# Kernel tuning notes

Measured on AMD Instinct MI355X. Metric: run time of the kernel, lower is better.

## Reference

```python
import jax, jax.numpy as jnp
import numpy as np

B, N, F, K = 16384, 64, 128, 64


def setup_inputs() -> dict:
    key = jax.random.key(0)
    kx, kd = jax.random.split(key)
    x = jax.random.normal(kx, (B, F), dtype=jnp.float32)
    D = jax.random.normal(kd, (N, F, K), dtype=jnp.float32)  # per-cluster factor dictionaries
    return {"x": x, "D": D}


def reference(x, D):
    # --- assignment step (torch.no_grad in original) ---
    # Dtx[n,b,j] = sum_i D[n,i,j] * x[b,i]
    Dtx = jnp.einsum('nij,bi->nbj', D, x)                      # [N,B,K]
    # per-cluster (D^T D)^{-1}, batched inverse over the cluster axis
    DTD = jnp.einsum('nij,nik->njk', D, D)                     # [N,K,K]
    DTD_inv = jnp.linalg.inv(DTD)                              # [N,K,K]
    Cs = jnp.einsum('nbj,nkj->nbk', Dtx, DTD_inv)              # [N,B,K]
    x_hat = jnp.einsum('nij,nbj->nbi', D, Cs)                  # [N,B,F]
    # nearest-subspace assignment per sample
    label = jnp.argmin(jnp.linalg.norm(x_hat - x[None], axis=-1), axis=0)  # [B] int
    C = Cs[label, jnp.arange(x.shape[0])]                      # [B,K] gather per sample
    # --- reconstruction loss: sum_i || x[i] - D[label[i]] @ C[i] ||^2 ---
    x_rec = jnp.einsum('bik,bk->bi', D[label], C)              # grouped gather + matmul
    se_loss = jnp.sum(jnp.square(x - x_rec))
    return se_loss, label
```

## Files before the change

### kernel.cpp

```cpp
#include <hip/hip_runtime.h>
#include <hip/hip_bf16.h>

#define B_N 16384
#define TAU 0.25f
#define GS 68
#define YS 132
#define DS 68

typedef float f32x4 __attribute__((ext_vector_type(4)));
typedef short s16x8 __attribute__((ext_vector_type(8)));

__device__ __forceinline__ void gl_lds16(const void* g, void* l) {
    __builtin_amdgcn_global_load_lds(
        (const __attribute__((address_space(1))) void*)g,
        (__attribute__((address_space(3))) void*)l, 16, 0, 0);
}

__device__ __forceinline__ unsigned short bf16_bits(float v) {
    __hip_bfloat16 h = __float2bfloat16(v);
    return *reinterpret_cast<unsigned short*>(&h);
}

__device__ __forceinline__ float readlane_f(float v, int l) {
    return __int_as_float(__builtin_amdgcn_readlane(__float_as_int(v), l));
}

__global__ __launch_bounds__(512) void prep_convert(const float* __restrict__ x,
                                                    const float* __restrict__ D,
                                                    unsigned short* __restrict__ xh,
                                                    float* __restrict__ nrm,
                                                    float* __restrict__ Qg,
                                                    unsigned short* __restrict__ Bht,
                                                    float* __restrict__ out) {
    const int t = threadIdx.x;

    if (blockIdx.x >= 64) {
        const int gid = (blockIdx.x - 64) * 512 + t;
        if (gid == 0) out[0] = 0.0f;
        const size_t base = (size_t)gid * 32;
        float s = 0.0f;
        #pragma unroll
        for (int c = 0; c < 8; ++c) {
            const f32x4 v = ((const f32x4*)(x + base))[c];
            s += v.x * v.x + v.y * v.y + v.z * v.z + v.w * v.w;
            ushort4 h;
            h.x = bf16_bits(v.x); h.y = bf16_bits(v.y);
            h.z = bf16_bits(v.z); h.w = bf16_bits(v.w);
            ((ushort4*)(xh + base))[c] = h;
        }
        s += __shfl_xor(s, 1, 64);
        s += __shfl_xor(s, 2, 64);
        if ((gid & 3) == 0) nrm[gid >> 2] = s;
        return;
    }

    __shared__ float Y[64 * YS];
    __shared__ __align__(16) float Dl[128 * DS];
    __shared__ __align__(16) float G[64 * GS + 64];
    __shared__ __align__(16) float Lti[8 * 8 * 8];
    const int n = blockIdx.x;
    const float* Dn = D + (size_t)n * 8192;

    for (int e4 = t; e4 < 2048; e4 += 512) {
        const int c = e4 >> 4, j4 = (e4 & 15) * 4;
        const f32x4 v = ((const f32x4*)Dn)[e4];
        *(f32x4*)&Dl[c * DS + j4] = v;
        Y[(j4 + 0) * YS + c] = v.x;
        Y[(j4 + 1) * YS + c] = v.y;
        Y[(j4 + 2) * YS + c] = v.z;
        Y[(j4 + 3) * YS + c] = v.w;
    }
    __syncthreads();

    {
        const int h = t >> 8;
        const int a0 = (t & 15) * 4, b0 = ((t >> 4) & 15) * 4;
        const int i0 = h * 64;
        float acc[4][4] = {};
        #pragma unroll 4
        for (int i = i0; i < i0 + 64; ++i) {
            const f32x4 av = *(const f32x4*)&Dl[i * DS + a0];
            const f32x4 bv = *(const f32x4*)&Dl[i * DS + b0];
            const float aa[4] = {av.x, av.y, av.z, av.w};
            const float bb[4] = {bv.x, bv.y, bv.z, bv.w};
            #pragma unroll
            for (int p = 0; p < 4; ++p)
                #pragma unroll
                for (int q = 0; q < 4; ++q) acc[p][q] = fmaf(aa[p], bb[q], acc[p][q]);
        }
        if (h == 0) {
            #pragma unroll
            for (int p = 0; p < 4; ++p)
                #pragma unroll
                for (int q = 0; q < 4; ++q) G[(a0 + p) * GS + b0 + q] = acc[p][q];
        }
        __syncthreads();
        if (h == 1) {
            #pragma unroll
            for (int p = 0; p < 4; ++p)
                #pragma unroll
                for (int q = 0; q < 4; ++q) G[(a0 + p) * GS + b0 + q] += acc[p][q];
        }
    }
    __syncthreads();

    #pragma unroll
    for (int p8 = 0; p8 < 8; ++p8) {
        const int pb = p8 * 8;
        if (t < 64) {
            const int lane = t;
            const f32x4 v0 = *(const f32x4*)&G[lane * GS + pb];
            const f32x4 v1 = *(const f32x4*)&G[lane * GS + pb + 4];
            float g[8] = {v0.x, v0.y, v0.z, v0.w, v1.x, v1.y, v1.z, v1.w};
            #pragma unroll
            for (int kk = 0; kk < 8; ++kk) {
                const int k = pb + kk;
                const float dk = readlane_f(g[kk], k);
                const float rinv = 1.0f / sqrtf(dk);
                const float lik = g[kk] * rinv;
                g[kk] = lik;
                if (lane == 0) G[64 * GS + k] = rinv;
                #pragma unroll
                for (int jj = kk + 1; jj < 8; ++jj) {
                    const float ljk = readlane_f(lik, pb + jj);
                    g[jj] -= lik * ljk;
                }
            }
            *(f32x4*)&G[lane * GS + pb]     = (f32x4){g[0], g[1], g[2], g[3]};
            *(f32x4*)&G[lane * GS + pb + 4] = (f32x4){g[4], g[5], g[6], g[7]};
        }
        __syncthreads();
        const int base = pb + 8;
        if (base < 64) {
            for (int i = base + (t >> 5); i < 64; i += 16) {
                const f32x4 Li0 = *(const f32x4*)&G[i * GS + pb];
                const f32x4 Li1 = *(const f32x4*)&G[i * GS + pb + 4];
                for (int j = base + (t & 31); j < 64; j += 32) {
                    const f32x4 Lj0 = *(const f32x4*)&G[j * GS + pb];
                    const f32x4 Lj1 = *(const f32x4*)&G[j * GS + pb + 4];
                    float s = G[i * GS + j];
                    s -= Li0.x * Lj0.x + Li0.y * Lj0.y + Li0.z * Lj0.z + Li0.w * Lj0.w;
                    s -= Li1.x * Lj1.x + Li1.y * Lj1.y + Li1.z * Lj1.z + Li1.w * Lj1.w;
                    G[i * GS + j] = s;
                }
            }
        }
        __syncthreads();
    }

    if (t < 64) {
        const int bi = t >> 3, c = t & 7;
        const int base = bi * 8;
        float m[8];
        #pragma unroll
        for (int r = 0; r < 8; ++r) {
            float s = (r == c) ? 1.0f : 0.0f;
            #pragma unroll
            for (int k = 0; k < r; ++k)
                s -= G[(base + r) * GS + base + k] * m[k];
            m[r] = s * G[64 * GS + base + r];
        }
        #pragma unroll
        for (int r = 0; r < 8; ++r) Lti[(base + r) * 8 + c] = m[r];
    }
    __syncthreads();

    {
        const int j = t >> 3, r = t & 7, jb = j >> 3;
        const float rinvj = G[64 * GS + j];
        for (int m8 = 0; m8 < 8; ++m8) {
            if (m8 >= jb) {
                const int g = m8 * 8 + r;
                float wv = (g == j) ? 1.0f : 0.0f;
                if (m8 > jb) {
                    #pragma unroll
                    for (int kk = 0; kk < 8; ++kk) {
                        const int gp = jb * 8 + kk;
                        const float liv = (gp > j) ? G[j * GS + gp]
                                         : ((gp == j) ? rinvj : 0.0f);
                        wv -= G[g * GS + gp] * liv;
                    }
                    for (int mm = jb + 1; mm < m8; ++mm) {
                        const f32x4 Lg0 = *(const f32x4*)&G[g * GS + mm * 8];
                        const f32x4 Lg1 = *(const f32x4*)&G[g * GS + mm * 8 + 4];
                        const f32x4 Mv0 = *(const f32x4*)&G[j * GS + mm * 8];
                        const f32x4 Mv1 = *(const f32x4*)&G[j * GS + mm * 8 + 4];
                        wv = fmaf(-Lg0.x, Mv0.x, wv);
                        wv = fmaf(-Lg0.y, Mv0.y, wv);
                        wv = fmaf(-Lg0.z, Mv0.z, wv);
                        wv = fmaf(-Lg0.w, Mv0.w, wv);
                        wv = fmaf(-Lg1.x, Mv1.x, wv);
                        wv = fmaf(-Lg1.y, Mv1.y, wv);
                        wv = fmaf(-Lg1.z, Mv1.z, wv);
                        wv = fmaf(-Lg1.w, Mv1.w, wv);
                    }
                }
                float z = 0.0f;
                #pragma unroll
                for (int rp = 0; rp < 8; ++rp) {
                    const float wrp = __shfl(wv, (t & 56) | rp, 64);
                    z = fmaf(Lti[g * 8 + rp], wrp, z);
                }
                if (g > j) G[j * GS + g] = z;
            }
            __syncthreads();
        }
    }

    {
        const int jj = t >> 5;
        const int jz = (jj & 1) ? (15 - (jj >> 1)) : (jj >> 1);
        const int j0 = jz * 4, c0 = (t & 31) * 4;
        const f32x4 rv4 = *(const f32x4*)&G[64 * GS + j0];
        float acc[4][4] = {};
        #pragma unroll 4
        for (int k = 0; k < j0; ++k) {
            const f32x4 lv = *(const f32x4*)&G[k * GS + j0];
            const f32x4 yv = *(const f32x4*)&Y[k * YS + c0];
            #pragma unroll
            for (int ej = 0; ej < 4; ++ej)
                #pragma unroll
                for (int ec = 0; ec < 4; ++ec)
                    acc[ej][ec] = fmaf(lv[ej], yv[ec], acc[ej][ec]);
        }
        #pragma unroll
        for (int kt = 0; kt < 4; ++kt) {
            const int k = j0 + kt;
            const f32x4 lq = *(const f32x4*)&G[k * GS + j0];
            const f32x4 yv = *(const f32x4*)&Y[k * YS + c0];
            #pragma unroll
            for (int ej = 0; ej < 4; ++ej) {
                const int jjj = j0 + ej;
                const float lsel = (jjj > k) ? lq[ej] : ((jjj == k) ? rv4[ej] : 0.0f);
                #pragma unroll
                for (int ec = 0; ec < 4; ++ec)
                    acc[ej][ec] = fmaf(lsel, yv[ec], acc[ej][ec]);
            }
        }
        #pragma unroll
        for (int ec = 0; ec < 4; ++ec) {
            *(f32x4*)&Qg[(size_t)n * 8192 + (c0 + ec) * 64 + j0] =
                (f32x4){acc[0][ec], acc[1][ec], acc[2][ec], acc[3][ec]};
        }
        #pragma unroll
        for (int ej = 0; ej < 4; ++ej) {
            ushort4 h;
            h.x = bf16_bits(acc[ej][0]); h.y = bf16_bits(acc[ej][1]);
            h.z = bf16_bits(acc[ej][2]); h.w = bf16_bits(acc[ej][3]);
            *(ushort4*)&Bht[((size_t)n * 64 + j0 + ej) * 128 + c0] = h;
        }
    }
}

__global__ __launch_bounds__(256) void gemm_argmax(const unsigned short* __restrict__ xh,
                                                   const unsigned short* __restrict__ Bht,
                                                   const float* __restrict__ nrm,
                                                   const float* __restrict__ x,
                                                   const float* __restrict__ Qg,
                                                   float* __restrict__ out) {
    __shared__ __align__(16) unsigned short ldsA[64 * 128];
    __shared__ __align__(16) unsigned short ldsB[2][64 * 128];
    __shared__ float scL[64 * 65];
    __shared__ float scPart[2][16][80];
    __shared__ int sflags[64];
    __shared__ int scnt;
    __shared__ float ssum;
    __shared__ float scorr[4];
    const int t = threadIdx.x, w = t >> 6, lane = t & 63;
    const int m0 = blockIdx.x * 64;
    const int lm = lane & 15, lg = lane >> 4;
    if (t == 0) scnt = 0;
    if (t < 4) scorr[t] = 0.0f;

    {
        const int rl = lane >> 4, p = lane & 15;
        #pragma unroll
        for (int q = 0; q < 4; ++q) {
            const int row = w * 16 + q * 4 + rl;
            const int c = p ^ (row & 15);
            gl_lds16(xh + (size_t)(m0 + row) * 128 + c * 8,
                     &ldsA[(w * 16 + q * 4) * 128]);
        }
        #pragma unroll
        for (int q = 0; q < 4; ++q) {
            const int row = w * 16 + q * 4 + rl;
            const int c = p ^ (row & 15);
            gl_lds16(Bht + (size_t)row * 128 + c * 8,
                     &ldsB[0][(w * 16 + q * 4) * 128]);
        }
    }
    __syncthreads();

    s16x8 bf[4][4];
    #pragma unroll
    for (int st = 0; st < 4; ++st) {
        const int r = st * 16 + lm;
        #pragma unroll
        for (int ks = 0; ks < 4; ++ks) {
            const int p = (ks * 4 + lg) ^ (r & 15);
            bf[st][ks] = *(const s16x8*)&ldsA[r * 128 + p * 8];
        }
    }

    float v1 = -1e30f, v2 = -1e30f;
    int n1 = 0;

    #pragma unroll 1
    for (int it = 0; it < 64; ++it) {
        const int cur = it & 1;

        s16x8 af[4];
        {
            const int r = w * 16 + lm;
            #pragma unroll
            for (int ks = 0; ks < 4; ++ks) {
                const int p = (ks * 4 + lg) ^ (r & 15);
                af[ks] = *(const s16x8*)&ldsB[cur][r * 128 + p * 8];
            }
        }

        if (it < 63) {
            const int rl = lane >> 4, p = lane & 15;
            #pragma unroll
            for (int q = 0; q < 4; ++q) {
                const int row = w * 16 + q * 4 + rl;
                const int c = p ^ (row & 15);
                gl_lds16(Bht + ((size_t)(it + 1) * 64 + row) * 128 + c * 8,
                         &ldsB[cur ^ 1][(w * 16 + q * 4) * 128]);
            }
        }

        #pragma unroll
        for (int st = 0; st < 4; ++st) {
            f32x4 acc = (f32x4){0.f, 0.f, 0.f, 0.f};
            #pragma unroll
            for (int ks = 0; ks < 4; ++ks)
                acc = __builtin_amdgcn_mfma_f32_16x16x32_bf16(af[ks], bf[st][ks], acc, 0, 0, 0);
            float q = acc[0] * acc[0];
            q = fmaf(acc[1], acc[1], q);
            q = fmaf(acc[2], acc[2], q);
            q = fmaf(acc[3], acc[3], q);
            scPart[cur][w * 4 + lg][st * 16 + lm] = q;
        }

        if (it > 0 && w == 0) {
            const int pb = cur ^ 1;
            float s = scPart[pb][0][lane];
            #pragma unroll
            for (int idx = 1; idx < 16; ++idx) s += scPart[pb][idx][lane];
            scL[lane * 65 + (it - 1)] = s;
            if (s > v1) { v2 = v1; v1 = s; n1 = it - 1; } else v2 = fmaxf(v2, s);
        }
        __syncthreads();
    }

    if (w == 0) {
        float s = scPart[1][0][lane];
        #pragma unroll
        for (int idx = 1; idx < 16; ++idx) s += scPart[1][idx][lane];
        scL[lane * 65 + 63] = s;
        if (s > v1) { v2 = v1; v1 = s; n1 = 63; } else v2 = fmaxf(v2, s);
        out[1 + m0 + lane] = (float)n1;
        if (v1 - v2 < TAU) { const int i = atomicAdd(&scnt, 1); sflags[i] = lane; }
        float err = nrm[m0 + lane] - v1;
        err += __shfl_xor(err, 1, 64);
        err += __shfl_xor(err, 2, 64);
        err += __shfl_xor(err, 4, 64);
        err += __shfl_xor(err, 8, 64);
        err += __shfl_xor(err, 16, 64);
        err += __shfl_xor(err, 32, 64);
        if (lane == 0) ssum = err;
    }
    __syncthreads();

    const int nf = scnt;
    float corr = 0.0f;
    for (int f = w; f < nf; f += 4) {
        const int s = sflags[f];
        const int b2 = m0 + s;
        const float v = scL[s * 65 + lane];
        float vm = v;
        for (int off = 32; off; off >>= 1) vm = fmaxf(vm, __shfl_xor(vm, off, 64));
        unsigned long long mask = __ballot((vm - v) < TAU);
        float best = -1e30f;
        int bn = 0;
        while (mask) {
            const int nn = (int)__builtin_ctzll(mask);
            mask &= mask - 1;
            const float* Qn = Qg + (size_t)nn * 8192;
            const float* xb = x + (size_t)b2 * 128;
            float d0 = 0.0f, d1 = 0.0f, d2 = 0.0f, d3 = 0.0f;
            #pragma unroll
            for (int i = 0; i < 128; i += 4) {
                d0 = fmaf(Qn[(i + 0) * 64 + lane], xb[i + 0], d0);
                d1 = fmaf(Qn[(i + 1) * 64 + lane], xb[i + 1], d1);
                d2 = fmaf(Qn[(i + 2) * 64 + lane], xb[i + 2], d2);
                d3 = fmaf(Qn[(i + 3) * 64 + lane], xb[i + 3], d3);
            }
            const float dot = (d0 + d1) + (d2 + d3);
            float sv = dot * dot;
            for (int off = 32; off; off >>= 1) sv += __shfl_xor(sv, off, 64);
            if (sv > best) { best = sv; bn = nn; }
        }
        if (lane == 0) {
            out[1 + b2] = (float)bn;
            corr += vm - best;
        }
    }
    if (lane == 0 && corr != 0.0f) scorr[w] += corr;
    __syncthreads();
    if (t == 0)
        atomicAdd(out, ssum + scorr[0] + scorr[1] + scorr[2] + scorr[3]);
}

extern "C" void kernel_launch(void* const* d_in, const int* in_sizes, int n_in,
                              void* d_out, int out_size, void* d_ws, size_t ws_size,
                              hipStream_t stream) {
    const float* x = (const float*)d_in[0];
    const float* D = (const float*)d_in[1];
    float* out = (float*)d_out;

    char* ws = (char*)d_ws;
    unsigned short* xh  = (unsigned short*)(ws);
    unsigned short* Bht = (unsigned short*)(ws + (4u << 20));
    float* Qg           = (float*)(ws + (5u << 20));
    float* nrm          = (float*)(ws + (11u << 20));

    prep_convert<<<192, 512, 0, stream>>>(x, D, xh, nrm, Qg, Bht, out);
    gemm_argmax<<<256, 256, 0, stream>>>(xh, Bht, nrm, x, Qg, out);
}
```

Baseline: 138.2 us.

## Triple-buffer B tiles with partial vmcnt waits and round-robin score reduction

Moves the B-tile staging in the argmax GEMM from double to triple buffering with a prefetch distance of two iterations. The full __syncthreads is replaced by a partial s_waitcnt vmcnt plus a raw s_barrier, so the next tile's loads stay in flight across the barrier. The per-iteration cross-wave score reduction now rotates across all four waves instead of always landing on wave 0, and a small merge step combines each wave's top-2 state at the end. To make room for the third buffer, the A tile and the score matrix share one LDS region, and scPart padding is trimmed. The hand-written waitcnt counts and the aliased LDS depend on exact load-issue ordering, which adds fragility.

```diff
diff --git a/kernel.cpp b/kernel.cpp
--- a/kernel.cpp
+++ b/kernel.cpp
@@ -258,36 +258,33 @@
                                                    const float* __restrict__ x,
                                                    const float* __restrict__ Qg,
                                                    float* __restrict__ out) {
-    __shared__ __align__(16) unsigned short ldsA[64 * 128];
-    __shared__ __align__(16) unsigned short ldsB[2][64 * 128];
-    __shared__ float scL[64 * 65];
-    __shared__ float scPart[2][16][80];
+    __shared__ __align__(16) unsigned short ldsB[3][64 * 128];
+    __shared__ __align__(16) unsigned char uniA[16704];
+    __shared__ float scPart[2][16][68];
     __shared__ int sflags[64];
     __shared__ int scnt;
     __shared__ float ssum;
     __shared__ float scorr[4];
+    unsigned short* ldsA = (unsigned short*)uniA;
+    float* scL = (float*)uniA;
+
     const int t = threadIdx.x, w = t >> 6, lane = t & 63;
     const int m0 = blockIdx.x * 64;
     const int lm = lane & 15, lg = lane >> 4;
+    const int rl = lane >> 4, sp = lane & 15;
     if (t == 0) scnt = 0;
     if (t < 4) scorr[t] = 0.0f;
 
-    {
-        const int rl = lane >> 4, p = lane & 15;
-        #pragma unroll
-        for (int q = 0; q < 4; ++q) {
-            const int row = w * 16 + q * 4 + rl;
-            const int c = p ^ (row & 15);
-            gl_lds16(xh + (size_t)(m0 + row) * 128 + c * 8,
-                     &ldsA[(w * 16 + q * 4) * 128]);
-        }
-        #pragma unroll
-        for (int q = 0; q < 4; ++q) {
-            const int row = w * 16 + q * 4 + rl;
-            const int c = p ^ (row & 15);
-            gl_lds16(Bht + (size_t)row * 128 + c * 8,
-                     &ldsB[0][(w * 16 + q * 4) * 128]);
-        }
+    #pragma unroll
+    for (int q = 0; q < 4; ++q) {
+        const int row = w * 16 + q * 4 + rl;
+        const int c = sp ^ (row & 15);
+        gl_lds16(xh + (size_t)(m0 + row) * 128 + c * 8,
+                 &ldsA[(w * 16 + q * 4) * 128]);
+        gl_lds16(Bht + (size_t)row * 128 + c * 8,
+                 &ldsB[0][(w * 16 + q * 4) * 128]);
+        gl_lds16(Bht + ((size_t)64 + row) * 128 + c * 8,
+                 &ldsB[1][(w * 16 + q * 4) * 128]);
     }
     __syncthreads();
 
@@ -307,7 +304,7 @@
 
     #pragma unroll 1
     for (int it = 0; it < 64; ++it) {
-        const int cur = it & 1;
+        const int cur = it % 3;
 
         s16x8 af[4];
         {
@@ -319,15 +316,24 @@
             }
         }
 
-        if (it < 63) {
-            const int rl = lane >> 4, p = lane & 15;
+        if (it < 62) {
+            const int nb = (it + 2) % 3;
             #pragma unroll
             for (int q = 0; q < 4; ++q) {
                 const int row = w * 16 + q * 4 + rl;
-                const int c = p ^ (row & 15);
-                gl_lds16(Bht + ((size_t)(it + 1) * 64 + row) * 128 + c * 8,
-                         &ldsB[cur ^ 1][(w * 16 + q * 4) * 128]);
-            }
+                const int c = sp ^ (row & 15);
+                gl_lds16(Bht + ((size_t)(it + 2) * 64 + row) * 128 + c * 8,
+                         &ldsB[nb][(w * 16 + q * 4) * 128]);
+            }
+        }
+
+        if (it > 0 && w == ((it - 1) & 3)) {
+            const int pb = (it - 1) & 1;
+            float s = scPart[pb][0][lane];
+            #pragma unroll
+            for (int idx = 1; idx < 16; ++idx) s += scPart[pb][idx][lane];
+            scL[lane * 65 + (it - 1)] = s;
+            if (s > v1) { v2 = v1; v1 = s; n1 = it - 1; } else v2 = fmaxf(v2, s);
         }
 
         #pragma unroll
@@ -340,29 +346,46 @@
             q = fmaf(acc[1], acc[1], q);
             q = fmaf(acc[2], acc[2], q);
             q = fmaf(acc[3], acc[3], q);
-            scPart[cur][w * 4 + lg][st * 16 + lm] = q;
-        }
-
-        if (it > 0 && w == 0) {
-            const int pb = cur ^ 1;
-            float s = scPart[pb][0][lane];
-            #pragma unroll
-            for (int idx = 1; idx < 16; ++idx) s += scPart[pb][idx][lane];
-            scL[lane * 65 + (it - 1)] = s;
-            if (s > v1) { v2 = v1; v1 = s; n1 = it - 1; } else v2 = fmaxf(v2, s);
-        }
-        __syncthreads();
-    }
-
-    if (w == 0) {
+            scPart[it & 1][w * 4 + lg][st * 16 + lm] = q;
+        }
+
+        if (it < 62) asm volatile("s_waitcnt vmcnt(4)" ::: "memory");
+        else         asm volatile("s_waitcnt vmcnt(0)" ::: "memory");
+        __builtin_amdgcn_s_barrier();
+        __builtin_amdgcn_sched_barrier(0);
+    }
+
+    if (w == 3) {
         float s = scPart[1][0][lane];
         #pragma unroll
         for (int idx = 1; idx < 16; ++idx) s += scPart[1][idx][lane];
         scL[lane * 65 + 63] = s;
         if (s > v1) { v2 = v1; v1 = s; n1 = 63; } else v2 = fmaxf(v2, s);
-        out[1 + m0 + lane] = (float)n1;
-        if (v1 - v2 < TAU) { const int i = atomicAdd(&scnt, 1); sflags[i] = lane; }
-        float err = nrm[m0 + lane] - v1;
+    }
+
+    {
+        float* mrg = &scPart[0][0][0];
+        mrg[w * 192 + lane]       = v1;
+        mrg[w * 192 + 64 + lane]  = v2;
+        mrg[w * 192 + 128 + lane] = (float)n1;
+    }
+    __syncthreads();
+
+    if (w == 0) {
+        const float* mrg = &scPart[0][0][0];
+        float b1 = -1e30f, b2 = -1e30f;
+        int bn = 0;
+        #pragma unroll
+        for (int ww = 0; ww < 4; ++ww) {
+            const float a1 = mrg[ww * 192 + lane];
+            const float a2 = mrg[ww * 192 + 64 + lane];
+            const int an = (int)mrg[ww * 192 + 128 + lane];
+            if (a1 > b1) { b2 = fmaxf(b1, a2); b1 = a1; bn = an; }
+            else b2 = fmaxf(b2, a1);
+        }
+        out[1 + m0 + lane] = (float)bn;
+        if (b1 - b2 < TAU) { const int i = atomicAdd(&scnt, 1); sflags[i] = lane; }
+        float err = nrm[m0 + lane] - b1;
         err += __shfl_xor(err, 1, 64);
         err += __shfl_xor(err, 2, 64);
         err += __shfl_xor(err, 4, 64);
```

Measured after the change: 140.5 us. No clear change (+1.7%).
